# Kernel tuning notes

Measured on AMD Instinct MI355X. Metric: run time of the kernel, lower is better.

Reference implementation:

```python
import jax, jax.numpy as jnp
import numpy as np

NEG_INF = -9e15  # matches the torch source's large-negative mask value
LRELU_SLOPE = 0.2


def setup_inputs() -> dict:
    key = jax.random.key(0)
    k1, k2, k3, k4, k5, k6 = jax.random.split(key, 6)
    N, D_IN, D_OUT = 8192, 512, 256
    h = jax.random.normal(k1, (N, D_IN), dtype=jnp.float32)
    adj = jax.random.randint(k2, (N, N), 0, 2, dtype=jnp.int32)
    # xavier_uniform with gain=1.414 for W [out, in] and a [1, 2*out]
    lim_W = 1.414 * np.sqrt(6.0 / (D_IN + D_OUT))
    lim_a = 1.414 * np.sqrt(6.0 / (2 * D_OUT + 1))
    W_w = jax.random.uniform(k3, (D_OUT, D_IN), minval=-lim_W, maxval=lim_W, dtype=jnp.float32)
    W_b = jax.random.normal(k4, (D_OUT,), dtype=jnp.float32) * 0.01
    a_w = jax.random.uniform(k5, (1, 2 * D_OUT), minval=-lim_a, maxval=lim_a, dtype=jnp.float32)
    a_b = jax.random.normal(k6, (1,), dtype=jnp.float32) * 0.01
    return {"h": h, "adj": adj, "W_w": W_w, "W_b": W_b, "a_w": a_w, "a_b": a_b}


def reference(h, adj, W_w, W_b, a_w, a_b):
    # wh = W(h): [N, d_out]
    wh = h @ W_w.T + W_b
    d_out = wh.shape[-1]
    # a(cat([wh_i, wh_j])) decomposes: a_src . wh_i + a_dst . wh_j + a_b
    # (identical math to the O(N^2 * 2d) repeat/cat in the torch source)
    a_src, a_dst = a_w[0, :d_out], a_w[0, d_out:]
    s_src = wh @ a_src  # [N]
    s_dst = wh @ a_dst  # [N]
    e = jax.nn.leaky_relu(s_src[:, None] + s_dst[None, :] + a_b[0], LRELU_SLOPE)  # [N, N]
    masked = jnp.where(adj > 0, e, jnp.float32(NEG_INF))
    attn = jax.nn.softmax(masked, axis=1)  # softmax over neighbors j
    return attn @ wh  # [N, d_out]
```

## Files before the change

### kernel.cpp

```cpp
#include <hip/hip_runtime.h>

typedef unsigned short ushort_t;
typedef unsigned int uint_t;
typedef __attribute__((ext_vector_type(8))) short short8;
typedef __attribute__((ext_vector_type(4))) float f32x4;
typedef __attribute__((ext_vector_type(4))) int i32x4;
typedef __attribute__((ext_vector_type(4))) uint_t u32x4;
typedef __attribute__((ext_vector_type(4))) ushort_t u16x4;

#define LRELU_SLOPE 0.2f

static __device__ __forceinline__ ushort_t f2bf(float f) {
    uint_t u = __builtin_bit_cast(uint_t, f);
    uint_t r = (u + 0x7fffu + ((u >> 16) & 1u)) >> 16;
    return (ushort_t)r;
}
static __device__ __forceinline__ uint4 pack8(float4 a, float4 b) {
    uint4 r;
    r.x = (uint_t)f2bf(a.x) | ((uint_t)f2bf(a.y) << 16);
    r.y = (uint_t)f2bf(a.z) | ((uint_t)f2bf(a.w) << 16);
    r.z = (uint_t)f2bf(b.x) | ((uint_t)f2bf(b.y) << 16);
    r.w = (uint_t)f2bf(b.z) | ((uint_t)f2bf(b.w) << 16);
    return r;
}

__launch_bounds__(256, 2)
__global__ void k1_gemm(const float* __restrict__ h, const float* __restrict__ W,
                        const float* __restrict__ Wb, const float* __restrict__ aw,
                        ushort_t* __restrict__ whB, float* __restrict__ s_src,
                        float* __restrict__ s_dst) {
    __shared__ __align__(16) ushort_t aT[256 * 72];
    __shared__ __align__(16) ushort_t bT[32 * 72];
    __shared__ float redLds[2][4][32];

    const int t = threadIdx.x;
    const int wv = t >> 6, ln = t & 63;
    const int i0 = blockIdx.x * 32;
    const int srow = t >> 3, sch = t & 7;
    const int row0 = ln & 15, kq = ln >> 4;

    f32x4 acc[4][2];
#pragma unroll
    for (int mt = 0; mt < 4; ++mt)
#pragma unroll
        for (int nt = 0; nt < 2; ++nt) acc[mt][nt] = (f32x4){0.f, 0.f, 0.f, 0.f};

    for (int k0 = 0; k0 < 512; k0 += 64) {
        __syncthreads();
#pragma unroll
        for (int r = 0; r < 8; ++r) {
            const float* gp = W + (size_t)(r * 32 + srow) * 512 + k0 + sch * 8;
            float4 x0 = *(const float4*)gp;
            float4 x1 = *(const float4*)(gp + 4);
            *(uint4*)(aT + (r * 32 + srow) * 72 + sch * 8) = pack8(x0, x1);
        }
        {
            const float* gp = h + (size_t)(i0 + srow) * 512 + k0 + sch * 8;
            float4 x0 = *(const float4*)gp;
            float4 x1 = *(const float4*)(gp + 4);
            *(uint4*)(bT + srow * 72 + sch * 8) = pack8(x0, x1);
        }
        __syncthreads();
#pragma unroll
        for (int ks = 0; ks < 2; ++ks) {
            short8 b[2];
#pragma unroll
            for (int nt = 0; nt < 2; ++nt)
                b[nt] = *(const short8*)(bT + (nt * 16 + row0) * 72 + ks * 32 + kq * 8);
#pragma unroll
            for (int mt = 0; mt < 4; ++mt) {
                short8 a = *(const short8*)(aT + (wv * 64 + mt * 16 + row0) * 72 + ks * 32 + kq * 8);
#pragma unroll
                for (int nt = 0; nt < 2; ++nt)
                    acc[mt][nt] = __builtin_amdgcn_mfma_f32_16x16x32_bf16(a, b[nt], acc[mt][nt], 0, 0, 0);
            }
        }
    }

    float psrc[2] = {0.f, 0.f}, pdst[2] = {0.f, 0.f};
#pragma unroll
    for (int mt = 0; mt < 4; ++mt) {
#pragma unroll
        for (int r = 0; r < 4; ++r) {
            const int o = wv * 64 + mt * 16 + (ln >> 4) * 4 + r;
            const float wbv = Wb[o];
            const float as = aw[o];
            const float ad = aw[256 + o];
#pragma unroll
            for (int nt = 0; nt < 2; ++nt) {
                const float v = acc[mt][nt][r] + wbv;
                psrc[nt] += v * as;
                pdst[nt] += v * ad;
                const int i = i0 + nt * 16 + (ln & 15);
                const int jt = i >> 6;
                const int khi = (i >> 5) & 1;
                const int kqi = (i >> 3) & 3;
                whB[((size_t)(jt * 2 + khi) * 256 + o) * 32 + kqi * 8 + (i & 7)] = f2bf(v);
            }
        }
    }
#pragma unroll
    for (int off = 16; off < 64; off <<= 1) {
#pragma unroll
        for (int nt = 0; nt < 2; ++nt) {
            psrc[nt] += __shfl_xor(psrc[nt], off, 64);
            pdst[nt] += __shfl_xor(pdst[nt], off, 64);
        }
    }
    if (ln < 16) {
#pragma unroll
        for (int nt = 0; nt < 2; ++nt) {
            redLds[0][wv][nt * 16 + ln] = psrc[nt];
            redLds[1][wv][nt * 16 + ln] = pdst[nt];
        }
    }
    __syncthreads();
    if (t < 32) {
        float s = 0.f;
#pragma unroll
        for (int w = 0; w < 4; ++w) s += redLds[0][w][t];
        s_src[i0 + t] = s;
    } else if (t < 64) {
        float s = 0.f;
#pragma unroll
        for (int w = 0; w < 4; ++w) s += redLds[1][w][t - 32];
        s_dst[i0 + t - 32] = s;
    }
}

__launch_bounds__(512, 4)
__global__ void k2_attn(const int* __restrict__ adj, const ushort_t* __restrict__ whB,
                        const float* __restrict__ s_src, const float* __restrict__ s_dst,
                        const float* __restrict__ ab_p, float* __restrict__ out0,
                        float* __restrict__ out1, float* __restrict__ zp, int jsplit) {
    __shared__ __align__(16) char smem[33792 + 128];
    ushort_t* pbuf = (ushort_t*)smem;
    float* exch = (float*)smem;
    float* zLds = (float*)(smem + 33792);

    const int t = threadIdx.x;
    const int wv = t >> 6, ln = t & 63;
    const int dq = wv & 3, kh = wv >> 2;
    const int row0 = ln & 15, kq = ln >> 4;
    const int split2 = (jsplit == 2);
    const int jb = split2 ? (int)(blockIdx.x & 1) : 0;
    const int ib = split2 ? (int)(blockIdx.x >> 1) : (int)blockIdx.x;
    const int i0 = ib * 32;
    const int jlen = split2 ? 4096 : 8192;
    const int jbase = jb * jlen;
    const int iters = jlen >> 6;
    const int prow = t >> 4, pjc = t & 15;

    const float ab = ab_p[0];
    const float ssrc = s_src[i0 + prow];

    const int* aBase = adj + (size_t)(i0 + prow) * 8192 + jbase + pjc * 4;
    const float* sBase = s_dst + jbase + pjc * 4;
    const ushort_t* bBase = whB + ((size_t)(jbase >> 6) * 2 + kh) * 8192
                            + (dq * 64 + row0) * 32 + kq * 8;

    f32x4 acc[2][4];
#pragma unroll
    for (int mt = 0; mt < 2; ++mt)
#pragma unroll
        for (int nt = 0; nt < 4; ++nt) acc[mt][nt] = (f32x4){0.f, 0.f, 0.f, 0.f};
    float zacc = 0.f;

    i32x4 Av = __builtin_nontemporal_load((const i32x4*)aBase);
    f32x4 Sv = *(const f32x4*)sBase;
    short8 Bv[4];
#pragma unroll
    for (int nt = 0; nt < 4; ++nt) Bv[nt] = *(const short8*)(bBase + nt * 512);

    for (int it = 0; it < iters; ++it) {
        const int itn = (it < iters - 1) ? it + 1 : it;
        const int jn = itn * 64;
        i32x4 Ac = Av;
        f32x4 Sc = Sv;
        short8 Bc[4];
#pragma unroll
        for (int nt = 0; nt < 4; ++nt) Bc[nt] = Bv[nt];
        Av = __builtin_nontemporal_load((const i32x4*)(aBase + jn));
        Sv = *(const f32x4*)(sBase + jn);
        {
            const ushort_t* bN = bBase + (size_t)itn * 16384;
#pragma unroll
            for (int nt = 0; nt < 4; ++nt) Bv[nt] = *(const short8*)(bN + nt * 512);
        }

        {
            u16x4 pv4;
            float z4 = 0.f;
#pragma unroll
            for (int k = 0; k < 4; ++k) {
                float sc = ssrc + Sc[k] + ab;
                sc = sc > 0.f ? sc : LRELU_SLOPE * sc;
                sc = fminf(sc, 60.f);
                float pv = (Ac[k] > 0) ? __expf(sc) : 0.f;
                z4 += pv;
                pv4[k] = f2bf(pv);
            }
            zacc += z4;
            *(u16x4*)(pbuf + (it & 1) * 2304 + prow * 72 + pjc * 4) = pv4;
        }
        __syncthreads();
        {
            const ushort_t* pc = pbuf + (it & 1) * 2304;
            short8 a0 = *(const short8*)(pc + row0 * 72 + kh * 32 + kq * 8);
            short8 a1 = *(const short8*)(pc + (16 + row0) * 72 + kh * 32 + kq * 8);
#pragma unroll
            for (int nt = 0; nt < 4; ++nt) {
                acc[0][nt] = __builtin_amdgcn_mfma_f32_16x16x32_bf16(a0, Bc[nt], acc[0][nt], 0, 0, 0);
                acc[1][nt] = __builtin_amdgcn_mfma_f32_16x16x32_bf16(a1, Bc[nt], acc[1][nt], 0, 0, 0);
            }
        }
    }

    zacc += __shfl_xor(zacc, 1, 64);
    zacc += __shfl_xor(zacc, 2, 64);
    zacc += __shfl_xor(zacc, 4, 64);
    zacc += __shfl_xor(zacc, 8, 64);
    if (split2) {
        if ((t & 15) == 0) zp[(size_t)jb * 8192 + i0 + prow] = zacc;
    } else {
        if ((t & 15) == 0) zLds[prow] = 1.0f / fmaxf(zacc, 1e-30f);
    }

    __syncthreads();
    if (kh == 1) {
        float* p = exch + (dq * 64 + ln) * 33;
#pragma unroll
        for (int mt = 0; mt < 2; ++mt)
#pragma unroll
            for (int nt = 0; nt < 4; ++nt)
#pragma unroll
                for (int r = 0; r < 4; ++r) p[mt * 16 + nt * 4 + r] = acc[mt][nt][r];
    }
    __syncthreads();
    if (kh == 0) {
        float* outp = (jb == 0) ? out0 : out1;
        const float* p = exch + (dq * 64 + ln) * 33;
#pragma unroll
        for (int mt = 0; mt < 2; ++mt)
#pragma unroll
            for (int nt = 0; nt < 4; ++nt)
#pragma unroll
                for (int r = 0; r < 4; ++r) {
                    const int il = mt * 16 + (ln >> 4) * 4 + r;
                    const int d = dq * 64 + nt * 16 + (ln & 15);
                    const float v = acc[mt][nt][r] + p[mt * 16 + nt * 4 + r];
                    if (split2)
                        outp[(size_t)(i0 + il) * 256 + d] = v;
                    else
                        outp[(size_t)(i0 + il) * 256 + d] = v * zLds[il];
                }
    }
}

__global__ void k3_norm(float* __restrict__ out, const float* __restrict__ part,
                        const float* __restrict__ zp) {
    const int i = blockIdx.x, t = threadIdx.x;
    const float rz = 1.0f / fmaxf(zp[i] + zp[8192 + i], 1e-30f);
    const size_t idx = (size_t)i * 256 + t;
    out[idx] = (out[idx] + part[idx]) * rz;
}

extern "C" void kernel_launch(void* const* d_in, const int* in_sizes, int n_in, void* d_out,
                              int out_size, void* d_ws, size_t ws_size, hipStream_t stream) {
    int order[16];
    for (int i = 0; i < n_in; ++i) order[i] = i;
    for (int a = 0; a < n_in; ++a)
        for (int b = a + 1; b < n_in; ++b)
            if (in_sizes[order[b]] < in_sizes[order[a]]) {
                int tmp = order[a]; order[a] = order[b]; order[b] = tmp;
            }
    const float* ab = (const float*)d_in[order[0]];
    const float* Wb = (const float*)d_in[order[1]];
    const float* aw = (const float*)d_in[order[2]];
    const float* Ww = (const float*)d_in[order[3]];
    const float* h = (const float*)d_in[order[4]];
    const int* adj = (const int*)d_in[order[5]];

    char* ws = (char*)d_ws;
    ushort_t* whB = (ushort_t*)ws;
    float* ssrc = (float*)(ws + 4194304);
    float* sdst = (float*)(ws + 4227072);
    float* part = (float*)(ws + 4259840);
    float* zp = (float*)(ws + 12648448);
    const size_t need = 12713984;
    const int jsplit = (ws_size >= need) ? 2 : 1;

    hipLaunchKernelGGL(k1_gemm, dim3(256), dim3(256), 0, stream, h, Ww, Wb, aw, whB, ssrc, sdst);
    hipLaunchKernelGGL(k2_attn, dim3(256 * jsplit), dim3(512), 0, stream, adj, whB, ssrc, sdst,
                       ab, (float*)d_out, part, zp, jsplit);
    if (jsplit == 2)
        hipLaunchKernelGGL(k3_norm, dim3(8192), dim3(256), 0, stream, (float*)d_out, part, zp);
}
```

Measured before the change: 432.2 us.

## Double attention row tile to 64 rows per block for B-operand reuse

Each attention block now processes 64 query rows instead of 32, computing two sets of masked exponentials and doing 4x4 MFMA tiles per step. This reuses each loaded wh B fragment across twice as many rows and halves the grid size. The cost is more registers and LDS (launch bounds drop to 2 blocks per CU), and fewer blocks in flight to hide adj streaming latency.

```diff
diff --git a/kernel.cpp b/kernel.cpp
--- a/kernel.cpp
+++ b/kernel.cpp
@@ -128,15 +128,15 @@
     }
 }
 
-__launch_bounds__(512, 4)
+__launch_bounds__(512, 2)
 __global__ void k2_attn(const int* __restrict__ adj, const ushort_t* __restrict__ whB,
                         const float* __restrict__ s_src, const float* __restrict__ s_dst,
                         const float* __restrict__ ab_p, float* __restrict__ out0,
                         float* __restrict__ out1, float* __restrict__ zp, int jsplit) {
-    __shared__ __align__(16) char smem[33792 + 128];
+    __shared__ __align__(16) char smem[66560 + 256];
     ushort_t* pbuf = (ushort_t*)smem;
     float* exch = (float*)smem;
-    float* zLds = (float*)(smem + 33792);
+    float* zLds = (float*)(smem + 66560);
 
     const int t = threadIdx.x;
     const int wv = t >> 6, ln = t & 63;
@@ -145,28 +145,31 @@
     const int split2 = (jsplit == 2);
     const int jb = split2 ? (int)(blockIdx.x & 1) : 0;
     const int ib = split2 ? (int)(blockIdx.x >> 1) : (int)blockIdx.x;
-    const int i0 = ib * 32;
+    const int i0 = ib * 64;
     const int jlen = split2 ? 4096 : 8192;
     const int jbase = jb * jlen;
     const int iters = jlen >> 6;
     const int prow = t >> 4, pjc = t & 15;
 
     const float ab = ab_p[0];
-    const float ssrc = s_src[i0 + prow];
-
-    const int* aBase = adj + (size_t)(i0 + prow) * 8192 + jbase + pjc * 4;
+    const float ssrc0 = s_src[i0 + prow];
+    const float ssrc1 = s_src[i0 + 32 + prow];
+
+    const int* aBase0 = adj + (size_t)(i0 + prow) * 8192 + jbase + pjc * 4;
+    const int* aBase1 = aBase0 + (size_t)32 * 8192;
     const float* sBase = s_dst + jbase + pjc * 4;
     const ushort_t* bBase = whB + ((size_t)(jbase >> 6) * 2 + kh) * 8192
                             + (dq * 64 + row0) * 32 + kq * 8;
 
-    f32x4 acc[2][4];
-#pragma unroll
-    for (int mt = 0; mt < 2; ++mt)
+    f32x4 acc[4][4];
+#pragma unroll
+    for (int mt = 0; mt < 4; ++mt)
 #pragma unroll
         for (int nt = 0; nt < 4; ++nt) acc[mt][nt] = (f32x4){0.f, 0.f, 0.f, 0.f};
-    float zacc = 0.f;
-
-    i32x4 Av = __builtin_nontemporal_load((const i32x4*)aBase);
+    float zacc0 = 0.f, zacc1 = 0.f;
+
+    i32x4 Av0 = __builtin_nontemporal_load((const i32x4*)aBase0);
+    i32x4 Av1 = __builtin_nontemporal_load((const i32x4*)aBase1);
     f32x4 Sv = *(const f32x4*)sBase;
     short8 Bv[4];
 #pragma unroll
@@ -175,12 +178,13 @@
     for (int it = 0; it < iters; ++it) {
         const int itn = (it < iters - 1) ? it + 1 : it;
         const int jn = itn * 64;
-        i32x4 Ac = Av;
+        i32x4 Ac0 = Av0, Ac1 = Av1;
         f32x4 Sc = Sv;
         short8 Bc[4];
 #pragma unroll
         for (int nt = 0; nt < 4; ++nt) Bc[nt] = Bv[nt];
-        Av = __builtin_nontemporal_load((const i32x4*)(aBase + jn));
+        Av0 = __builtin_nontemporal_load((const i32x4*)(aBase0 + jn));
+        Av1 = __builtin_nontemporal_load((const i32x4*)(aBase1 + jn));
         Sv = *(const f32x4*)(sBase + jn);
         {
             const ushort_t* bN = bBase + (size_t)itn * 16384;
@@ -189,48 +193,69 @@
         }
 
         {
+            ushort_t* pc = pbuf + (it & 1) * 4608;
             u16x4 pv4;
             float z4 = 0.f;
 #pragma unroll
             for (int k = 0; k < 4; ++k) {
-                float sc = ssrc + Sc[k] + ab;
+                float sc = ssrc0 + Sc[k] + ab;
                 sc = sc > 0.f ? sc : LRELU_SLOPE * sc;
                 sc = fminf(sc, 60.f);
-                float pv = (Ac[k] > 0) ? __expf(sc) : 0.f;
+                float pv = (Ac0[k] > 0) ? __expf(sc) : 0.f;
                 z4 += pv;
                 pv4[k] = f2bf(pv);
             }
-            zacc += z4;
-            *(u16x4*)(pbuf + (it & 1) * 2304 + prow * 72 + pjc * 4) = pv4;
+            zacc0 += z4;
+            *(u16x4*)(pc + prow * 72 + pjc * 4) = pv4;
+            z4 = 0.f;
+#pragma unroll
+            for (int k = 0; k < 4; ++k) {
+                float sc = ssrc1 + Sc[k] + ab;
+                sc = sc > 0.f ? sc : LRELU_SLOPE * sc;
+                sc = fminf(sc, 60.f);
+                float pv = (Ac1[k] > 0) ? __expf(sc) : 0.f;
+                z4 += pv;
+                pv4[k] = f2bf(pv);
+            }
+            zacc1 += z4;
+            *(u16x4*)(pc + (32 + prow) * 72 + pjc * 4) = pv4;
         }
         __syncthreads();
         {
-            const ushort_t* pc = pbuf + (it & 1) * 2304;
-            short8 a0 = *(const short8*)(pc + row0 * 72 + kh * 32 + kq * 8);
-            short8 a1 = *(const short8*)(pc + (16 + row0) * 72 + kh * 32 + kq * 8);
-#pragma unroll
-            for (int nt = 0; nt < 4; ++nt) {
-                acc[0][nt] = __builtin_amdgcn_mfma_f32_16x16x32_bf16(a0, Bc[nt], acc[0][nt], 0, 0, 0);
-                acc[1][nt] = __builtin_amdgcn_mfma_f32_16x16x32_bf16(a1, Bc[nt], acc[1][nt], 0, 0, 0);
-            }
-        }
-    }
-
-    zacc += __shfl_xor(zacc, 1, 64);
-    zacc += __shfl_xor(zacc, 2, 64);
-    zacc += __shfl_xor(zacc, 4, 64);
-    zacc += __shfl_xor(zacc, 8, 64);
-    if (split2) {
-        if ((t & 15) == 0) zp[(size_t)jb * 8192 + i0 + prow] = zacc;
-    } else {
-        if ((t & 15) == 0) zLds[prow] = 1.0f / fmaxf(zacc, 1e-30f);
+            const ushort_t* pc = pbuf + (it & 1) * 4608;
+#pragma unroll
+            for (int mt = 0; mt < 4; ++mt) {
+                short8 a = *(const short8*)(pc + (mt * 16 + row0) * 72 + kh * 32 + kq * 8);
+#pragma unroll
+                for (int nt = 0; nt < 4; ++nt)
+                    acc[mt][nt] = __builtin_amdgcn_mfma_f32_16x16x32_bf16(a, Bc[nt], acc[mt][nt], 0, 0, 0);
+            }
+        }
+    }
+
+    zacc0 += __shfl_xor(zacc0, 1, 64);
+    zacc1 += __shfl_xor(zacc1, 1, 64);
+    zacc0 += __shfl_xor(zacc0, 2, 64);
+    zacc1 += __shfl_xor(zacc1, 2, 64);
+    zacc0 += __shfl_xor(zacc0, 4, 64);
+    zacc1 += __shfl_xor(zacc1, 4, 64);
+    zacc0 += __shfl_xor(zacc0, 8, 64);
+    zacc1 += __shfl_xor(zacc1, 8, 64);
+    if ((t & 15) == 0) {
+        if (split2) {
+            zp[(size_t)jb * 8192 + i0 + prow] = zacc0;
+            zp[(size_t)jb * 8192 + i0 + 32 + prow] = zacc1;
+        } else {
+            zLds[prow] = 1.0f / fmaxf(zacc0, 1e-30f);
+            zLds[32 + prow] = 1.0f / fmaxf(zacc1, 1e-30f);
+        }
     }
 
     __syncthreads();
     if (kh == 1) {
-        float* p = exch + (dq * 64 + ln) * 33;
-#pragma unroll
-        for (int mt = 0; mt < 2; ++mt)
+        float* p = exch + (dq * 64 + ln) * 65;
+#pragma unroll
+        for (int mt = 0; mt < 4; ++mt)
 #pragma unroll
             for (int nt = 0; nt < 4; ++nt)
 #pragma unroll
@@ -239,9 +264,9 @@
     __syncthreads();
     if (kh == 0) {
         float* outp = (jb == 0) ? out0 : out1;
-        const float* p = exch + (dq * 64 + ln) * 33;
-#pragma unroll
-        for (int mt = 0; mt < 2; ++mt)
+        const float* p = exch + (dq * 64 + ln) * 65;
+#pragma unroll
+        for (int mt = 0; mt < 4; ++mt)
 #pragma unroll
             for (int nt = 0; nt < 4; ++nt)
 #pragma unroll
@@ -291,7 +316,7 @@
     const int jsplit = (ws_size >= need) ? 2 : 1;
 
     hipLaunchKernelGGL(k1_gemm, dim3(256), dim3(256), 0, stream, h, Ww, Wb, aw, whB, ssrc, sdst);
-    hipLaunchKernelGGL(k2_attn, dim3(256 * jsplit), dim3(512), 0, stream, adj, whB, ssrc, sdst,
+    hipLaunchKernelGGL(k2_attn, dim3(128 * jsplit), dim3(512), 0, stream, adj, whB, ssrc, sdst,
                        ab, (float*)d_out, part, zp, jsplit);
     if (jsplit == 2)
         hipLaunchKernelGGL(k3_norm, dim3(8192), dim3(256), 0, stream, (float*)d_out, part, zp);
```

After: 418.6 us. -3.2%, faster.
